# Kernel optimization log

Hardware: AMD Instinct MI355X
Metric: run time of the kernel (lower is better)

## Reference

```python
import jax, jax.numpy as jnp
import numpy as np

MAX_DIST = 5
D_PE = 16
NUM_ENTITIES = 50000
NUM_EDGES = 800000
NUM_ANCHOR_TRIPLES = 32
MAX_SOURCES = 2 * NUM_ANCHOR_TRIPLES  # upper bound on unique anchor entities


def setup_inputs() -> dict:
    key = jax.random.key(0)
    k1, k2, k3, k4 = jax.random.split(key, 4)
    h_ids = jax.random.randint(k1, (NUM_EDGES,), 0, NUM_ENTITIES)
    t_ids = jax.random.randint(k2, (NUM_EDGES,), 0, NUM_ENTITIES)
    anchor_triple_indices = jax.random.randint(k3, (NUM_ANCHOR_TRIPLES,), 0, NUM_EDGES)
    dist_embed = jax.random.normal(k4, (MAX_DIST + 1, D_PE), dtype=jnp.float32)
    return {
        "h_ids": h_ids,
        "t_ids": t_ids,
        "anchor_triple_indices": anchor_triple_indices,
        "num_entities": NUM_ENTITIES,
        "dist_embed": dist_embed,
    }


def _bfs_mean_counts(h_ids, t_ids, anchor_triple_indices, num_entities):
    """Returns [num_entities, MAX_DIST+1] mean one-hot distance counts over anchors."""
    # unique anchor entities, padded with -1 to a static size (torch.unique equivalent)
    anchor_ents = jnp.concatenate([h_ids[anchor_triple_indices], t_ids[anchor_triple_indices]])
    sources = jnp.unique(anchor_ents, size=MAX_SOURCES, fill_value=-1)  # [K], sorted
    valid = sources >= 0                                                # [K]
    src = jnp.where(valid, sources, 0)
    K = src.shape[0]
    col = jnp.arange(K)

    # symmetric adjacency as edge list (duplicates are harmless: only >0 is tested)
    edge_src = jnp.concatenate([h_ids, t_ids])  # [2E]
    edge_dst = jnp.concatenate([t_ids, h_ids])  # [2E]

    frontier = jnp.zeros((num_entities, K), jnp.float32).at[src, col].set(1.0)
    visited = jnp.zeros((num_entities, K), bool).at[src, col].set(True)
    dist = jnp.full((num_entities, K), MAX_DIST, jnp.int32).at[src, col].set(0)

    for depth in range(1, MAX_DIST + 1):  # fixed small hop count
        # sparse adj @ frontier == scatter-add of gathered frontier rows
        new_frontier = jax.ops.segment_sum(frontier[edge_src], edge_dst, num_segments=num_entities)
        newly = (new_frontier > 0) & ~visited
        dist = jnp.where(newly, depth, dist)
        visited = visited | newly
        frontier = newly.astype(jnp.float32)

    # masked mean over valid anchor sources, expressed as distance-count histogram
    w = valid.astype(jnp.float32)
    n_valid = jnp.maximum(w.sum(), 1.0)
    onehot = jax.nn.one_hot(dist, MAX_DIST + 1, dtype=jnp.float32)  # [N, K, D+1]
    counts = jnp.einsum('nkd,k->nd', onehot, w) / n_valid           # [N, D+1]
    return counts


def reference(h_ids, t_ids, anchor_triple_indices, num_entities, dist_embed):
    counts = _bfs_mean_counts(h_ids, t_ids, anchor_triple_indices, num_entities)
    # mean over sources of embed(dist) == counts @ embedding table
    return counts @ dist_embed  # [num_entities, d_pe]
```

## Files before the change

kernel.cpp:

```cpp
#include <hip/hip_runtime.h>

typedef unsigned long long u64;
typedef unsigned int u32;

#define MAXD 5
#define NTH  256
#define BN   64
#define BIN_SH 9
#define BIN_NODES 512
#define SL   16
#define CAPB 24576
#define HEMPTY 0xFFFFFFFFu


__global__ void anchors_k(const int* __restrict__ h, const int* __restrict__ t,
                          const int* __restrict__ anchor, int A,
                          u64* __restrict__ V0, int* __restrict__ nvalid) {
    int tid = threadIdx.x;
    int K = 2 * A;
    int a_ = (tid < K) ? anchor[(tid < A) ? tid : (tid - A)] : 0;
    int my = (tid < K) ? ((tid < A) ? h[a_] : t[a_]) : -1;
    bool uniq = (tid < K);
    for (int j = 0; j < 64; ++j) {
        int o = __shfl(my, j, 64);
        if (j < tid && o == my) uniq = false;
    }
    u64 mask = __ballot(uniq);
    if (tid == 0) *nvalid = (int)__popcll(mask);
    if (uniq) V0[my] = 1ull << tid;
}

__global__ __launch_bounds__(NTH) void sortA(
    const int* __restrict__ h, const int* __restrict__ t, int E, int NBIN,
    u32* __restrict__ binCur, u32* __restrict__ binBuf) {
    __shared__ u32 hist[128], base[128];
    __shared__ u32 offs[129];
    __shared__ u32 buf[4096];
    int tid = threadIdx.x, b = blockIdx.x;
    int e0 = b * 4 * NTH * 2 / 2;
    e0 = b * 2048;
    u32 eu[8], ev[8];
#pragma unroll
    for (int k = 0; k < 8; ++k) {
        int i = e0 + k * NTH + tid;
        if (i < E) {
            eu[k] = (u32)__builtin_nontemporal_load(h + i);
            ev[k] = (u32)__builtin_nontemporal_load(t + i);
        } else { eu[k] = HEMPTY; ev[k] = HEMPTY; }
    }
    for (int i = tid; i < NBIN; i += NTH) hist[i] = 0u;
    __syncthreads();
#pragma unroll
    for (int k = 0; k < 8; ++k) {
        if (eu[k] != HEMPTY) {
            atomicAdd(&hist[ev[k] >> BIN_SH], 1u);
            atomicAdd(&hist[eu[k] >> BIN_SH], 1u);
        }
    }
    __syncthreads();
    if (tid == 0) {
        u32 s = 0;
        for (int j = 0; j < NBIN; ++j) { offs[j] = s; s += hist[j]; }
        offs[NBIN] = s;
    }
    __syncthreads();
    if (tid < NBIN) {
        u32 c = offs[tid + 1] - offs[tid];
        base[tid] = c ? atomicAdd(&binCur[tid], c) : 0u;
        hist[tid] = 0u;
    }
    __syncthreads();
#pragma unroll
    for (int k = 0; k < 8; ++k) {
        if (eu[k] != HEMPTY) {
            u32 b1 = ev[k] >> BIN_SH;
            buf[offs[b1] + atomicAdd(&hist[b1], 1u)] =
                (eu[k] << BIN_SH) | (ev[k] & (BIN_NODES - 1));
            u32 b2 = eu[k] >> BIN_SH;
            buf[offs[b2] + atomicAdd(&hist[b2], 1u)] =
                (ev[k] << BIN_SH) | (eu[k] & (BIN_NODES - 1));
        }
    }
    __syncthreads();
    u32 tot = offs[NBIN];
    for (u32 i = tid; i < tot; i += NTH) {
        int c = 0;
#pragma unroll
        for (int step = 64; step >= 1; step >>= 1)
            if (c + step <= NBIN - 1 && offs[c + step] <= i) c += step;
        u32 pos = base[c] + (i - offs[c]);
        if (pos < CAPB) binBuf[(size_t)c * CAPB + pos] = buf[i];
    }
}

__global__ __launch_bounds__(NTH) void pull_k(
    const u32* __restrict__ binBuf, const u32* __restrict__ binCur,
    const u64* __restrict__ Fin, u64* __restrict__ P, int NP) {
    __shared__ u64 NF[BIN_NODES];
    int bin = blockIdx.x >> 4, sl = blockIdx.x & (SL - 1);
    int tid = threadIdx.x;
    for (int j = tid; j < BIN_NODES; j += NTH) NF[j] = 0ull;
    __syncthreads();
    u32 cnt = min(binCur[bin], (u32)CAPB);
    u32 per = (cnt + SL - 1) / SL;
    u32 r0 = min((u32)sl * per, cnt), r1 = min(r0 + per, cnt);
    const u32* rb = binBuf + (size_t)bin * CAPB;
    u32 r = r0 + tid;
    for (; r + 3u * NTH < r1; r += 4u * NTH) {
        u32 a0 = __builtin_nontemporal_load(rb + r);
        u32 a1 = __builtin_nontemporal_load(rb + r + NTH);
        u32 a2 = __builtin_nontemporal_load(rb + r + 2 * NTH);
        u32 a3 = __builtin_nontemporal_load(rb + r + 3 * NTH);
        u64 f0 = Fin[a0 >> BIN_SH], f1 = Fin[a1 >> BIN_SH];
        u64 f2 = Fin[a2 >> BIN_SH], f3 = Fin[a3 >> BIN_SH];
        if (f0) atomicOr(&NF[a0 & (BIN_NODES - 1)], f0);
        if (f1) atomicOr(&NF[a1 & (BIN_NODES - 1)], f1);
        if (f2) atomicOr(&NF[a2 & (BIN_NODES - 1)], f2);
        if (f3) atomicOr(&NF[a3 & (BIN_NODES - 1)], f3);
    }
    for (; r < r1; r += NTH) {
        u32 a0 = __builtin_nontemporal_load(rb + r);
        u64 f0 = Fin[a0 >> BIN_SH];
        if (f0) atomicOr(&NF[a0 & (BIN_NODES - 1)], f0);
    }
    __syncthreads();
    u64* Pd = P + (size_t)sl * NP + ((size_t)bin << BIN_SH);
    for (int j = tid; j < BIN_NODES; j += NTH) Pd[j] = NF[j];
}

__global__ __launch_bounds__(NTH) void combine1_k(
    const u64* __restrict__ P, int NP, const u64* __restrict__ V0,
    u64* __restrict__ NF1, u64* __restrict__ Vis, int N) {
    int n = blockIdx.x * NTH + threadIdx.x;
    if (n >= N) return;
    u64 raw = 0ull;
#pragma unroll
    for (int s = 0; s < SL; ++s) raw |= P[(size_t)s * NP + n];
    u64 v0 = V0[n];
    u64 nw = raw & ~v0;
    NF1[n] = nw;
    Vis[n] = v0 | nw;
}

__global__ __launch_bounds__(NTH) void combine_k(
    const u64* __restrict__ P, int NP,
    u64* __restrict__ NFk, u64* __restrict__ Vis, int N) {
    int n = blockIdx.x * NTH + threadIdx.x;
    if (n >= N) return;
    u64 raw = 0ull;
#pragma unroll
    for (int s = 0; s < SL; ++s) raw |= P[(size_t)s * NP + n];
    u64 vis = Vis[n];
    u64 nw = raw & ~vis;
    NFk[n] = nw;
    Vis[n] = vis | nw;
}

__global__ __launch_bounds__(NTH) void final_k(
    const u64* __restrict__ P, int NP, const u64* __restrict__ V0,
    const u64* __restrict__ NF1, const u64* __restrict__ NF2,
    const u64* __restrict__ NF3, const u64* __restrict__ Vis,
    const int* __restrict__ nvalid, const float* __restrict__ embed,
    float* __restrict__ out, int N) {
    __shared__ float cds[BN][8];
    int b = blockIdx.x, tid = threadIdx.x;
    int nv = *nvalid;
    if (tid < BN) {
        int n = b * BN + tid;
        if (n < N) {
            u64 raw = 0ull;
#pragma unroll
            for (int s = 0; s < SL; ++s) raw |= P[(size_t)s * NP + n];
            u64 n4 = raw & ~Vis[n];
            int c0 = V0[n] ? 1 : 0;
            int c1 = __popcll(NF1[n]), c2 = __popcll(NF2[n]);
            int c3 = __popcll(NF3[n]), c4 = __popcll(n4);
            cds[tid][0] = (float)c0; cds[tid][1] = (float)c1;
            cds[tid][2] = (float)c2; cds[tid][3] = (float)c3;
            cds[tid][4] = (float)c4;
            cds[tid][5] = (float)(nv - (c0 + c1 + c2 + c3 + c4));
        }
    }
    __syncthreads();
    int nl = tid >> 2, q = tid & 3;
    int n = b * BN + nl;
    if (n >= N) return;
    float inv = 1.0f / (float)(nv > 0 ? nv : 1);
    const float4* e4 = (const float4*)embed;
    float4 acc = {0.f, 0.f, 0.f, 0.f};
#pragma unroll
    for (int d = 0; d <= MAXD; ++d) {
        float cd = cds[nl][d];
        float4 e = e4[d * 4 + q];
        acc.x += cd * e.x; acc.y += cd * e.y;
        acc.z += cd * e.z; acc.w += cd * e.w;
    }
    acc.x *= inv; acc.y *= inv; acc.z *= inv; acc.w *= inv;
    ((float4*)(out + (size_t)n * 16))[q] = acc;
}

extern "C" void kernel_launch(void* const* d_in, const int* in_sizes, int n_in,
                              void* d_out, int out_size, void* d_ws, size_t ws_size,
                              hipStream_t stream) {
    const int*   h      = (const int*)d_in[0];
    const int*   t      = (const int*)d_in[1];
    const int*   anchor = (const int*)d_in[2];
    const float* embed  = (const float*)d_in[4];
    float*       out    = (float*)d_out;

    int E = in_sizes[0];
    int A = in_sizes[2];
    int D = in_sizes[4] / (MAXD + 1);
    int N = out_size / D;
    int NBIN = (N + BIN_NODES - 1) >> BIN_SH;
    int NP   = NBIN << BIN_SH;
    int NBs  = (E + 2047) / 2048;
    int NBc  = (N + NTH - 1) / NTH;
    int NBf  = (N + BN - 1) / BN;
    (void)D;

    u64* V0     = (u64*)d_ws;
    u32* binCur = (u32*)(V0 + N);
    int* nvalid = (int*)(binCur + 128);
    u64* Vis    = (u64*)((char*)d_ws + (((size_t)N * 8 + 128 * 4 + 16 + 15) & ~(size_t)15));
    u64* NF1    = Vis + N;
    u64* NF2    = NF1 + N;
    u64* NF3    = NF2 + N;
    u64* P      = NF3 + N;
    u32* binBuf = (u32*)(P + (size_t)SL * NP);

    hipMemsetAsync(V0, 0, (size_t)N * 8 + 128 * 4 + 16, stream);

    anchors_k<<<1, 64, 0, stream>>>(h, t, anchor, A, V0, nvalid);
    sortA<<<NBs, NTH, 0, stream>>>(h, t, E, NBIN, binCur, binBuf);

    pull_k<<<NBIN * SL, NTH, 0, stream>>>(binBuf, binCur, V0, P, NP);
    combine1_k<<<NBc, NTH, 0, stream>>>(P, NP, V0, NF1, Vis, N);

    pull_k<<<NBIN * SL, NTH, 0, stream>>>(binBuf, binCur, NF1, P, NP);
    combine_k<<<NBc, NTH, 0, stream>>>(P, NP, NF2, Vis, N);

    pull_k<<<NBIN * SL, NTH, 0, stream>>>(binBuf, binCur, NF2, P, NP);
    combine_k<<<NBc, NTH, 0, stream>>>(P, NP, NF3, Vis, N);

    pull_k<<<NBIN * SL, NTH, 0, stream>>>(binBuf, binCur, NF3, P, NP);
    final_k<<<NBf, NTH, 0, stream>>>(P, NP, V0, NF1, NF2, NF3, Vis,
                                     nvalid, embed, out, N);
}
```

Baseline: 152.6 us.

## Fuse BFS combine steps into pull kernels with smaller 128-node bins

```diff
diff --git a/kernel.cpp b/kernel.cpp
--- a/kernel.cpp
+++ b/kernel.cpp
@@ -5,40 +5,24 @@
 
 #define MAXD 5
 #define NTH  256
-#define BN   64
-#define BIN_SH 9
-#define BIN_NODES 512
-#define SL   16
-#define CAPB 24576
+#define BIN_SH 7
+#define BIN_NODES 128
+#define MAXBIN 512
+#define CAPB 5120
+#define EPB  2048
 #define HEMPTY 0xFFFFFFFFu
 
-
-__global__ void anchors_k(const int* __restrict__ h, const int* __restrict__ t,
-                          const int* __restrict__ anchor, int A,
-                          u64* __restrict__ V0, int* __restrict__ nvalid) {
-    int tid = threadIdx.x;
-    int K = 2 * A;
-    int a_ = (tid < K) ? anchor[(tid < A) ? tid : (tid - A)] : 0;
-    int my = (tid < K) ? ((tid < A) ? h[a_] : t[a_]) : -1;
-    bool uniq = (tid < K);
-    for (int j = 0; j < 64; ++j) {
-        int o = __shfl(my, j, 64);
-        if (j < tid && o == my) uniq = false;
-    }
-    u64 mask = __ballot(uniq);
-    if (tid == 0) *nvalid = (int)__popcll(mask);
-    if (uniq) V0[my] = 1ull << tid;
-}
 
 __global__ __launch_bounds__(NTH) void sortA(
     const int* __restrict__ h, const int* __restrict__ t, int E, int NBIN,
     u32* __restrict__ binCur, u32* __restrict__ binBuf) {
-    __shared__ u32 hist[128], base[128];
-    __shared__ u32 offs[129];
-    __shared__ u32 buf[4096];
+    __shared__ u32 hist[MAXBIN], base[MAXBIN];
+    __shared__ u32 offs[MAXBIN + 1];
+    __shared__ u32 waveSum[4];
+    __shared__ u32 buf[2 * EPB];
     int tid = threadIdx.x, b = blockIdx.x;
-    int e0 = b * 4 * NTH * 2 / 2;
-    e0 = b * 2048;
+    int lane = tid & 63, w = tid >> 6;
+    int e0 = b * EPB;
     u32 eu[8], ev[8];
 #pragma unroll
     for (int k = 0; k < 8; ++k) {
@@ -58,16 +42,32 @@
         }
     }
     __syncthreads();
-    if (tid == 0) {
-        u32 s = 0;
-        for (int j = 0; j < NBIN; ++j) { offs[j] = s; s += hist[j]; }
-        offs[NBIN] = s;
-    }
-    __syncthreads();
-    if (tid < NBIN) {
-        u32 c = offs[tid + 1] - offs[tid];
-        base[tid] = c ? atomicAdd(&binCur[tid], c) : 0u;
-        hist[tid] = 0u;
+    {
+        u32 i0 = (u32)tid * 2;
+        u32 a0 = (i0 < (u32)NBIN) ? hist[i0] : 0u;
+        u32 a1 = (i0 + 1 < (u32)NBIN) ? hist[i0 + 1] : 0u;
+        u32 sum = a0 + a1;
+        u32 p = sum;
+#pragma unroll
+        for (int d = 1; d < 64; d <<= 1) {
+            u32 x = (u32)__shfl_up((int)p, d, 64);
+            if (lane >= d) p += x;
+        }
+        u32 excl = p - sum;
+        if (lane == 63) waveSum[w] = p;
+        __syncthreads();
+        u32 woff = 0;
+        for (int k = 0; k < w; ++k) woff += waveSum[k];
+        u32 o0 = woff + excl;
+        if (i0 < (u32)NBIN) offs[i0] = o0;
+        if (i0 + 1 < (u32)NBIN) offs[i0 + 1] = o0 + a0;
+        if (tid == NTH - 1) offs[NBIN] = o0 + a0 + a1;
+    }
+    __syncthreads();
+    for (int j = tid; j < NBIN; j += NTH) {
+        u32 c = offs[j + 1] - offs[j];
+        base[j] = c ? atomicAdd(&binCur[j], c) : 0u;
+        hist[j] = 0u;
     }
     __syncthreads();
 #pragma unroll
@@ -86,95 +86,173 @@
     for (u32 i = tid; i < tot; i += NTH) {
         int c = 0;
 #pragma unroll
-        for (int step = 64; step >= 1; step >>= 1)
+        for (int step = 256; step >= 1; step >>= 1)
             if (c + step <= NBIN - 1 && offs[c + step] <= i) c += step;
         u32 pos = base[c] + (i - offs[c]);
         if (pos < CAPB) binBuf[(size_t)c * CAPB + pos] = buf[i];
     }
 }
 
-__global__ __launch_bounds__(NTH) void pull_k(
+__global__ __launch_bounds__(NTH) void pull1(
     const u32* __restrict__ binBuf, const u32* __restrict__ binCur,
-    const u64* __restrict__ Fin, u64* __restrict__ P, int NP) {
+    const int* __restrict__ h, const int* __restrict__ t,
+    const int* __restrict__ anchor, int A,
+    u64* __restrict__ F1, u64* __restrict__ Vis, u64* __restrict__ CNT,
+    int N) {
     __shared__ u64 NF[BIN_NODES];
-    int bin = blockIdx.x >> 4, sl = blockIdx.x & (SL - 1);
-    int tid = threadIdx.x;
-    for (int j = tid; j < BIN_NODES; j += NTH) NF[j] = 0ull;
-    __syncthreads();
+    __shared__ u32 hsKey[128], hsBit[128];
+    int tid = threadIdx.x, bin = blockIdx.x;
+    if (tid < 128) { NF[tid & (BIN_NODES - 1)] = 0ull; hsKey[tid] = HEMPTY; }
+    __syncthreads();
+    if (tid < 64) {
+        int K = 2 * A;
+        int a_ = (tid < K) ? anchor[(tid < A) ? tid : (tid - A)] : 0;
+        int my = (tid < K) ? ((tid < A) ? h[a_] : t[a_]) : -1;
+        bool uniq = (tid < K);
+        for (int j = 0; j < 64; ++j) {
+            int o = __shfl(my, j, 64);
+            if (j < tid && o == my) uniq = false;
+        }
+        if (uniq) {
+            u32 slot = ((u32)my * 2654435761u) >> 25;
+            while (atomicCAS(&hsKey[slot], HEMPTY, (u32)my) != HEMPTY)
+                slot = (slot + 1) & 127u;
+            hsBit[slot] = (u32)tid;
+        }
+    }
+    __syncthreads();
+    auto srcMask = [&](u32 src) -> u64 {
+        u32 slot = (src * 2654435761u) >> 25;
+        while (true) {
+            u32 k = hsKey[slot];
+            if (k == src) return 1ull << hsBit[slot];
+            if (k == HEMPTY) return 0ull;
+            slot = (slot + 1) & 127u;
+        }
+    };
     u32 cnt = min(binCur[bin], (u32)CAPB);
-    u32 per = (cnt + SL - 1) / SL;
-    u32 r0 = min((u32)sl * per, cnt), r1 = min(r0 + per, cnt);
     const u32* rb = binBuf + (size_t)bin * CAPB;
-    u32 r = r0 + tid;
-    for (; r + 3u * NTH < r1; r += 4u * NTH) {
-        u32 a0 = __builtin_nontemporal_load(rb + r);
-        u32 a1 = __builtin_nontemporal_load(rb + r + NTH);
-        u32 a2 = __builtin_nontemporal_load(rb + r + 2 * NTH);
-        u32 a3 = __builtin_nontemporal_load(rb + r + 3 * NTH);
-        u64 f0 = Fin[a0 >> BIN_SH], f1 = Fin[a1 >> BIN_SH];
-        u64 f2 = Fin[a2 >> BIN_SH], f3 = Fin[a3 >> BIN_SH];
+    const uint4* rb4 = (const uint4*)rb;
+    u32 n4 = cnt >> 2;
+    for (u32 i = tid; i < n4; i += NTH) {
+        uint4 rr = rb4[i];
+        u64 f0 = srcMask(rr.x >> BIN_SH), f1 = srcMask(rr.y >> BIN_SH);
+        u64 f2 = srcMask(rr.z >> BIN_SH), f3 = srcMask(rr.w >> BIN_SH);
+        if (f0) atomicOr(&NF[rr.x & (BIN_NODES - 1)], f0);
+        if (f1) atomicOr(&NF[rr.y & (BIN_NODES - 1)], f1);
+        if (f2) atomicOr(&NF[rr.z & (BIN_NODES - 1)], f2);
+        if (f3) atomicOr(&NF[rr.w & (BIN_NODES - 1)], f3);
+    }
+    for (u32 r = (n4 << 2) + tid; r < cnt; r += NTH) {
+        u32 a0 = rb[r];
+        u64 f0 = srcMask(a0 >> BIN_SH);
         if (f0) atomicOr(&NF[a0 & (BIN_NODES - 1)], f0);
-        if (f1) atomicOr(&NF[a1 & (BIN_NODES - 1)], f1);
-        if (f2) atomicOr(&NF[a2 & (BIN_NODES - 1)], f2);
-        if (f3) atomicOr(&NF[a3 & (BIN_NODES - 1)], f3);
-    }
-    for (; r < r1; r += NTH) {
-        u32 a0 = __builtin_nontemporal_load(rb + r);
+    }
+    __syncthreads();
+    if (tid < BIN_NODES) {
+        int n = bin * BIN_NODES + tid;
+        if (n < N) {
+            u64 srcbit = srcMask((u32)n);
+            u64 nw = NF[tid] & ~srcbit;
+            F1[n] = nw;
+            Vis[n] = srcbit | nw;
+            CNT[n] = (srcbit ? 1ull : 0ull) | ((u64)__popcll(nw) << 8);
+        }
+    }
+}
+
+__global__ __launch_bounds__(NTH) void pull_mid(
+    const u32* __restrict__ binBuf, const u32* __restrict__ binCur,
+    const u64* __restrict__ Fin, u64* __restrict__ Fout,
+    u64* __restrict__ Vis, u64* __restrict__ CNT, int shift, int N) {
+    __shared__ u64 NF[BIN_NODES];
+    int tid = threadIdx.x, bin = blockIdx.x;
+    if (tid < BIN_NODES) NF[tid] = 0ull;
+    __syncthreads();
+    u32 cnt = min(binCur[bin], (u32)CAPB);
+    const u32* rb = binBuf + (size_t)bin * CAPB;
+    const uint4* rb4 = (const uint4*)rb;
+    u32 n4 = cnt >> 2;
+    for (u32 i = tid; i < n4; i += NTH) {
+        uint4 rr = rb4[i];
+        u64 f0 = Fin[rr.x >> BIN_SH], f1 = Fin[rr.y >> BIN_SH];
+        u64 f2 = Fin[rr.z >> BIN_SH], f3 = Fin[rr.w >> BIN_SH];
+        if (f0) atomicOr(&NF[rr.x & (BIN_NODES - 1)], f0);
+        if (f1) atomicOr(&NF[rr.y & (BIN_NODES - 1)], f1);
+        if (f2) atomicOr(&NF[rr.z & (BIN_NODES - 1)], f2);
+        if (f3) atomicOr(&NF[rr.w & (BIN_NODES - 1)], f3);
+    }
+    for (u32 r = (n4 << 2) + tid; r < cnt; r += NTH) {
+        u32 a0 = rb[r];
         u64 f0 = Fin[a0 >> BIN_SH];
         if (f0) atomicOr(&NF[a0 & (BIN_NODES - 1)], f0);
     }
     __syncthreads();
-    u64* Pd = P + (size_t)sl * NP + ((size_t)bin << BIN_SH);
-    for (int j = tid; j < BIN_NODES; j += NTH) Pd[j] = NF[j];
-}
-
-__global__ __launch_bounds__(NTH) void combine1_k(
-    const u64* __restrict__ P, int NP, const u64* __restrict__ V0,
-    u64* __restrict__ NF1, u64* __restrict__ Vis, int N) {
-    int n = blockIdx.x * NTH + threadIdx.x;
-    if (n >= N) return;
-    u64 raw = 0ull;
-#pragma unroll
-    for (int s = 0; s < SL; ++s) raw |= P[(size_t)s * NP + n];
-    u64 v0 = V0[n];
-    u64 nw = raw & ~v0;
-    NF1[n] = nw;
-    Vis[n] = v0 | nw;
-}
-
-__global__ __launch_bounds__(NTH) void combine_k(
-    const u64* __restrict__ P, int NP,
-    u64* __restrict__ NFk, u64* __restrict__ Vis, int N) {
-    int n = blockIdx.x * NTH + threadIdx.x;
-    if (n >= N) return;
-    u64 raw = 0ull;
-#pragma unroll
-    for (int s = 0; s < SL; ++s) raw |= P[(size_t)s * NP + n];
-    u64 vis = Vis[n];
-    u64 nw = raw & ~vis;
-    NFk[n] = nw;
-    Vis[n] = vis | nw;
-}
-
-__global__ __launch_bounds__(NTH) void final_k(
-    const u64* __restrict__ P, int NP, const u64* __restrict__ V0,
-    const u64* __restrict__ NF1, const u64* __restrict__ NF2,
-    const u64* __restrict__ NF3, const u64* __restrict__ Vis,
-    const int* __restrict__ nvalid, const float* __restrict__ embed,
-    float* __restrict__ out, int N) {
-    __shared__ float cds[BN][8];
-    int b = blockIdx.x, tid = threadIdx.x;
-    int nv = *nvalid;
-    if (tid < BN) {
-        int n = b * BN + tid;
+    if (tid < BIN_NODES) {
+        int n = bin * BIN_NODES + tid;
         if (n < N) {
-            u64 raw = 0ull;
-#pragma unroll
-            for (int s = 0; s < SL; ++s) raw |= P[(size_t)s * NP + n];
-            u64 n4 = raw & ~Vis[n];
-            int c0 = V0[n] ? 1 : 0;
-            int c1 = __popcll(NF1[n]), c2 = __popcll(NF2[n]);
-            int c3 = __popcll(NF3[n]), c4 = __popcll(n4);
+            u64 vis = Vis[n];
+            u64 nw = NF[tid] & ~vis;
+            Fout[n] = nw;
+            Vis[n] = vis | nw;
+            CNT[n] += (u64)__popcll(nw) << shift;
+        }
+    }
+}
+
+__global__ __launch_bounds__(NTH) void pull4fin(
+    const u32* __restrict__ binBuf, const u32* __restrict__ binCur,
+    const u64* __restrict__ Fin, const u64* __restrict__ Vis,
+    const u64* __restrict__ CNT,
+    const int* __restrict__ h, const int* __restrict__ t,
+    const int* __restrict__ anchor, int A,
+    const float* __restrict__ embed, float* __restrict__ out, int N) {
+    __shared__ u64 NF[BIN_NODES];
+    __shared__ float cds[BIN_NODES][8];
+    __shared__ int nvs;
+    int tid = threadIdx.x, bin = blockIdx.x;
+    if (tid < BIN_NODES) NF[tid] = 0ull;
+    if (tid < 64) {
+        int K = 2 * A;
+        int a_ = (tid < K) ? anchor[(tid < A) ? tid : (tid - A)] : 0;
+        int my = (tid < K) ? ((tid < A) ? h[a_] : t[a_]) : -1;
+        bool uniq = (tid < K);
+        for (int j = 0; j < 64; ++j) {
+            int o = __shfl(my, j, 64);
+            if (j < tid && o == my) uniq = false;
+        }
+        u64 mask = __ballot(uniq);
+        if (tid == 0) nvs = (int)__popcll(mask);
+    }
+    __syncthreads();
+    u32 cnt = min(binCur[bin], (u32)CAPB);
+    const u32* rb = binBuf + (size_t)bin * CAPB;
+    const uint4* rb4 = (const uint4*)rb;
+    u32 n4 = cnt >> 2;
+    for (u32 i = tid; i < n4; i += NTH) {
+        uint4 rr = rb4[i];
+        u64 f0 = Fin[rr.x >> BIN_SH], f1 = Fin[rr.y >> BIN_SH];
+        u64 f2 = Fin[rr.z >> BIN_SH], f3 = Fin[rr.w >> BIN_SH];
+        if (f0) atomicOr(&NF[rr.x & (BIN_NODES - 1)], f0);
+        if (f1) atomicOr(&NF[rr.y & (BIN_NODES - 1)], f1);
+        if (f2) atomicOr(&NF[rr.z & (BIN_NODES - 1)], f2);
+        if (f3) atomicOr(&NF[rr.w & (BIN_NODES - 1)], f3);
+    }
+    for (u32 r = (n4 << 2) + tid; r < cnt; r += NTH) {
+        u32 a0 = rb[r];
+        u64 f0 = Fin[a0 >> BIN_SH];
+        if (f0) atomicOr(&NF[a0 & (BIN_NODES - 1)], f0);
+    }
+    __syncthreads();
+    int nv = nvs;
+    if (tid < BIN_NODES) {
+        int n = bin * BIN_NODES + tid;
+        if (n < N) {
+            u64 nw4 = NF[tid] & ~Vis[n];
+            u64 c = CNT[n];
+            int c0 = (int)(c & 0xffull), c1 = (int)((c >> 8) & 0xffull);
+            int c2 = (int)((c >> 16) & 0xffull), c3 = (int)((c >> 24) & 0xffull);
+            int c4 = __popcll(nw4);
             cds[tid][0] = (float)c0; cds[tid][1] = (float)c1;
             cds[tid][2] = (float)c2; cds[tid][3] = (float)c3;
             cds[tid][4] = (float)c4;
@@ -182,21 +260,25 @@
         }
     }
     __syncthreads();
-    int nl = tid >> 2, q = tid & 3;
-    int n = b * BN + nl;
+    int nl = tid >> 1, q = tid & 1;
+    int n = bin * BIN_NODES + nl;
     if (n >= N) return;
     float inv = 1.0f / (float)(nv > 0 ? nv : 1);
     const float4* e4 = (const float4*)embed;
-    float4 acc = {0.f, 0.f, 0.f, 0.f};
+    float4 accA = {0.f, 0.f, 0.f, 0.f}, accB = {0.f, 0.f, 0.f, 0.f};
 #pragma unroll
     for (int d = 0; d <= MAXD; ++d) {
         float cd = cds[nl][d];
-        float4 e = e4[d * 4 + q];
-        acc.x += cd * e.x; acc.y += cd * e.y;
-        acc.z += cd * e.z; acc.w += cd * e.w;
-    }
-    acc.x *= inv; acc.y *= inv; acc.z *= inv; acc.w *= inv;
-    ((float4*)(out + (size_t)n * 16))[q] = acc;
+        float4 ea = e4[d * 4 + q * 2], eb = e4[d * 4 + q * 2 + 1];
+        accA.x += cd * ea.x; accA.y += cd * ea.y;
+        accA.z += cd * ea.z; accA.w += cd * ea.w;
+        accB.x += cd * eb.x; accB.y += cd * eb.y;
+        accB.z += cd * eb.z; accB.w += cd * eb.w;
+    }
+    accA.x *= inv; accA.y *= inv; accA.z *= inv; accA.w *= inv;
+    accB.x *= inv; accB.y *= inv; accB.z *= inv; accB.w *= inv;
+    float4* o4 = (float4*)(out + (size_t)n * 16);
+    o4[q * 2] = accA; o4[q * 2 + 1] = accB;
 }
 
 extern "C" void kernel_launch(void* const* d_in, const int* in_sizes, int n_in,
@@ -213,37 +295,23 @@
     int D = in_sizes[4] / (MAXD + 1);
     int N = out_size / D;
     int NBIN = (N + BIN_NODES - 1) >> BIN_SH;
-    int NP   = NBIN << BIN_SH;
-    int NBs  = (E + 2047) / 2048;
-    int NBc  = (N + NTH - 1) / NTH;
-    int NBf  = (N + BN - 1) / BN;
+    int NBs  = (E + EPB - 1) / EPB;
     (void)D;
 
-    u64* V0     = (u64*)d_ws;
-    u32* binCur = (u32*)(V0 + N);
-    int* nvalid = (int*)(binCur + 128);
-    u64* Vis    = (u64*)((char*)d_ws + (((size_t)N * 8 + 128 * 4 + 16 + 15) & ~(size_t)15));
-    u64* NF1    = Vis + N;
-    u64* NF2    = NF1 + N;
-    u64* NF3    = NF2 + N;
-    u64* P      = NF3 + N;
-    u32* binBuf = (u32*)(P + (size_t)SL * NP);
-
-    hipMemsetAsync(V0, 0, (size_t)N * 8 + 128 * 4 + 16, stream);
-
-    anchors_k<<<1, 64, 0, stream>>>(h, t, anchor, A, V0, nvalid);
+    u32* binCur = (u32*)d_ws;
+    u64* Vis    = (u64*)(binCur + 512);
+    u64* Fa     = Vis + N;
+    u64* Fb     = Fa + N;
+    u64* CNT    = Fb + N;
+    u32* binBuf = (u32*)(CNT + N);
+
+    hipMemsetAsync(binCur, 0, 512 * 4, stream);
+
     sortA<<<NBs, NTH, 0, stream>>>(h, t, E, NBIN, binCur, binBuf);
-
-    pull_k<<<NBIN * SL, NTH, 0, stream>>>(binBuf, binCur, V0, P, NP);
-    combine1_k<<<NBc, NTH, 0, stream>>>(P, NP, V0, NF1, Vis, N);
-
-    pull_k<<<NBIN * SL, NTH, 0, stream>>>(binBuf, binCur, NF1, P, NP);
-    combine_k<<<NBc, NTH, 0, stream>>>(P, NP, NF2, Vis, N);
-
-    pull_k<<<NBIN * SL, NTH, 0, stream>>>(binBuf, binCur, NF2, P, NP);
-    combine_k<<<NBc, NTH, 0, stream>>>(P, NP, NF3, Vis, N);
-
-    pull_k<<<NBIN * SL, NTH, 0, stream>>>(binBuf, binCur, NF3, P, NP);
-    final_k<<<NBf, NTH, 0, stream>>>(P, NP, V0, NF1, NF2, NF3, Vis,
-                                     nvalid, embed, out, N);
-}
+    pull1<<<NBIN, NTH, 0, stream>>>(binBuf, binCur, h, t, anchor, A,
+                                    Fa, Vis, CNT, N);
+    pull_mid<<<NBIN, NTH, 0, stream>>>(binBuf, binCur, Fa, Fb, Vis, CNT, 16, N);
+    pull_mid<<<NBIN, NTH, 0, stream>>>(binBuf, binCur, Fb, Fa, Vis, CNT, 24, N);
+    pull4fin<<<NBIN, NTH, 0, stream>>>(binBuf, binCur, Fa, Vis, CNT,
+                                       h, t, anchor, A, embed, out, N);
+}
```

New measurement: 147.8 us. 3.1% less time.
